# Performance work log

Hardware: AMD Instinct MI355X
Metric: run time of the kernel (lower is better)

The kernel has to match this reference:

```python
import jax, jax.numpy as jnp
import numpy as np

B, C, H, W = 4, 256, 64, 64
CQ = C // 8


def setup_inputs() -> dict:
    key = jax.random.key(0)
    ks = jax.random.split(key, 7)
    x = jax.random.normal(ks[0], (B, C, H, W), dtype=jnp.float32)
    Wq = jax.random.normal(ks[1], (CQ, C), dtype=jnp.float32) * 0.02
    bq = jnp.zeros((CQ,), dtype=jnp.float32)
    Wk = jax.random.normal(ks[2], (CQ, C), dtype=jnp.float32) * 0.02
    bk = jnp.zeros((CQ,), dtype=jnp.float32)
    Wv = jax.random.normal(ks[3], (C, C), dtype=jnp.float32) * 0.02
    bv = jnp.zeros((C,), dtype=jnp.float32)
    return {"x": x, "Wq": Wq, "bq": bq, "Wk": Wk, "bk": bk, "Wv": Wv, "bv": bv}


def reference(x, Wq, bq, Wk, bk, Wv, bv):
    b, c, h, w = x.shape
    n = h * w
    xf = x.reshape(b, c, n)                                   # [B,C,N]
    # 1x1 convs are per-pixel GEMMs
    q = jnp.einsum('qc,bcn->bnq', Wq, xf) + bq                # [B,N,Cq]
    k = jnp.einsum('qc,bcn->bqn', Wk, xf) + bk[None, :, None] # [B,Cq,N]
    v = jnp.einsum('vc,bcn->bnv', Wv, xf) + bv                # [B,N,C]
    scale = float(n) ** 0.5
    energy = jnp.einsum('bnq,bqm->bnm', q, k) / scale         # [B,N,N]
    attn = jax.nn.softmax(energy, axis=-1)
    out = jnp.einsum('bnm,bmv->bnv', attn, v)                 # [B,N,C]
    # Faithful to torch's out.view(B,C,H,W) applied to the contiguous [B,N,C]
    # tensor: a raw memory reinterpretation, NOT a transpose.
    return out.reshape(b, c, h, w)
```

## Files before the change

### kernel.cpp

```cpp
#include <hip/hip_runtime.h>

#define BATCH 4
#define CH    256
#define NPIX  4096
#define CQD   32

typedef __bf16 bf16;
typedef bf16 bf16x8 __attribute__((ext_vector_type(8)));
typedef bf16 bf16x4 __attribute__((ext_vector_type(4)));
typedef float f32x4 __attribute__((ext_vector_type(4)));

#define MFMA16 __builtin_amdgcn_mfma_f32_16x16x32_bf16

__global__ __launch_bounds__(256) void proj_kernel(
    const float* __restrict__ x,
    const float* __restrict__ Wq, const float* __restrict__ bq,
    const float* __restrict__ Wk, const float* __restrict__ bk,
    const float* __restrict__ Wv, const float* __restrict__ bv,
    bf16* __restrict__ qp, bf16* __restrict__ kp, bf16* __restrict__ vT)
{
    __shared__ __align__(16) bf16 xT[32][264];
    __shared__ __align__(16) bf16 vstage[4][16][40];

    const int t  = threadIdx.x;
    const int b  = blockIdx.x >> 7;
    const int n0 = (blockIdx.x & 127) << 5;
    const int w    = t >> 6;
    const int lane = t & 63;
    const int l16  = t & 15;
    const int quad = (t & 63) >> 4;

    auto params = [&](int rt, const float*& Wp, const float*& bp, float& scale,
                      int& rbase, int& kind) {
        int ro = w * 80 + rt * 16;
        if (ro < 32)      { Wp = Wq; bp = bq; scale = 0.015625f; rbase = ro;      kind = 0; }
        else if (ro < 64) { Wp = Wk; bp = bk; scale = 1.0f;      rbase = ro - 32; kind = 1; }
        else              { Wp = Wv; bp = bv; scale = 1.0f;      rbase = ro - 64; kind = 2; }
    };

    const float* Wp; const float* bp; float scale; int rbase; int kind;
    params(0, Wp, bp, scale, rbase, kind);
    float4 wraw[16];
    {
        const float* wrow = Wp + (size_t)(rbase + l16) * CH + quad * 8;
#pragma unroll
        for (int kc = 0; kc < 8; ++kc) {
            wraw[2 * kc]     = *(const float4*)(wrow + kc * 32);
            wraw[2 * kc + 1] = *(const float4*)(wrow + kc * 32 + 4);
        }
    }

    const float* xb = x + (size_t)b * CH * NPIX;
#pragma unroll
    for (int j = 0; j < 8; ++j) {
        int id = t + j * 256;
        int c  = id >> 3;
        int n4 = (id & 7) << 2;
        float4 vv = *(const float4*)(xb + (size_t)c * NPIX + n0 + n4);
        xT[n4 + 0][c] = (bf16)vv.x;
        xT[n4 + 1][c] = (bf16)vv.y;
        xT[n4 + 2][c] = (bf16)vv.z;
        xT[n4 + 3][c] = (bf16)vv.w;
    }
    __syncthreads();

    for (int rt = 0; rt < 5; ++rt) {
        bf16x8 afrag[8];
#pragma unroll
        for (int kc = 0; kc < 8; ++kc) {
            float4 wa = wraw[2 * kc], wb = wraw[2 * kc + 1];
            bf16x8 a;
            a[0] = (bf16)wa.x; a[1] = (bf16)wa.y; a[2] = (bf16)wa.z; a[3] = (bf16)wa.w;
            a[4] = (bf16)wb.x; a[5] = (bf16)wb.y; a[6] = (bf16)wb.z; a[7] = (bf16)wb.w;
            afrag[kc] = a;
        }
        const float* Wp2; const float* bp2; float scale2; int rbase2; int kind2;
        if (rt < 4) {
            params(rt + 1, Wp2, bp2, scale2, rbase2, kind2);
            const float* wrow = Wp2 + (size_t)(rbase2 + l16) * CH + quad * 8;
#pragma unroll
            for (int kc = 0; kc < 8; ++kc) {
                wraw[2 * kc]     = *(const float4*)(wrow + kc * 32);
                wraw[2 * kc + 1] = *(const float4*)(wrow + kc * 32 + 4);
            }
        }
        float bv4[4];
#pragma unroll
        for (int r = 0; r < 4; ++r) bv4[r] = bp[rbase + quad * 4 + r];

#pragma unroll
        for (int nt = 0; nt < 2; ++nt) {
            f32x4 acc = {0.f, 0.f, 0.f, 0.f};
#pragma unroll
            for (int kc = 0; kc < 8; ++kc) {
                bf16x8 bfr = *(const bf16x8*)&xT[nt * 16 + l16][kc * 32 + quad * 8];
                acc = MFMA16(afrag[kc], bfr, acc, 0, 0, 0);
            }
            if (kind != 2) {
                bf16x4 pk;
#pragma unroll
                for (int r = 0; r < 4; ++r)
                    pk[r] = (bf16)((acc[r] + bv4[r]) * scale);
                int n = n0 + nt * 16 + l16;
                bf16* dst = (kind == 0) ? qp : kp;
                *(bf16x4*)&dst[((size_t)b * NPIX + n) * CQD + rbase + quad * 4] = pk;
            } else {
#pragma unroll
                for (int r = 0; r < 4; ++r)
                    vstage[w][quad * 4 + r][nt * 16 + l16] = (bf16)(acc[r] + bv4[r]);
            }
        }
        if (kind == 2) {
            int vrow = lane >> 2, vcc = lane & 3;
            bf16x8 chunk = *(const bf16x8*)&vstage[w][vrow][vcc * 8];
            *(bf16x8*)&vT[((size_t)b * CH + rbase + vrow) * NPIX + n0 + vcc * 8] = chunk;
        }
        if (rt < 4) { Wp = Wp2; bp = bp2; scale = scale2; rbase = rbase2; kind = kind2; }
    }
}

template<int S, bool DIRECT>
__global__ __launch_bounds__(256, 2) void attn_kernel(
    const bf16* __restrict__ qp, const bf16* __restrict__ kp,
    const bf16* __restrict__ vT,
    bf16* __restrict__ Opart, float* __restrict__ Lpart,
    float* __restrict__ out)
{
    __shared__ __align__(16) bf16 Kt[64][40];
    __shared__ __align__(16) bf16 Vt[256][64];
    __shared__ __align__(16) bf16 Pb[4][16][72];

    const int t    = threadIdx.x;
    const int bid  = blockIdx.x;
    const int s    = bid % S;
    const int tq   = bid / S;
    const int b    = tq >> 5;
    const int qt   = tq & 31;
    const int n0   = qt << 7;
    const int w    = t >> 6;
    const int lane = t & 63;
    const int l16  = t & 15;
    const int quad = (t & 63) >> 4;

    const bf16* qpb = qp + ((size_t)b * NPIX + n0 + w * 32) * CQD;
    bf16x8 qfrag[2];
    qfrag[0] = *(const bf16x8*)(qpb + (size_t)l16 * CQD + quad * 8);
    qfrag[1] = *(const bf16x8*)(qpb + (size_t)(16 + l16) * CQD + quad * 8);

    f32x4 o[2][16];
#pragma unroll
    for (int g = 0; g < 2; ++g)
#pragma unroll
        for (int ct = 0; ct < 16; ++ct) o[g][ct] = (f32x4){0.f, 0.f, 0.f, 0.f};
    float lsum[2] = {0.f, 0.f};

    const bf16* kpb = kp + (size_t)b * NPIX * CQD;
    const bf16* vTb = vT + (size_t)b * CH * NPIX;
    const int k0 = s * (NPIX / S);
    const int sw = l16 & 7;

    for (int mi = 0; mi < NPIX / S / 64; ++mi) {
        const int m0 = k0 + (mi << 6);
        {
            int row = t >> 2, cc = t & 3;
            *(bf16x8*)&Kt[row][cc * 8] =
                *(const bf16x8*)(kpb + (size_t)(m0 + row) * CQD + cc * 8);
        }
#pragma unroll
        for (int j = 0; j < 8; ++j) {
            int id  = t + j * 256;
            int row = id >> 3, cc = id & 7;
            *(bf16x8*)&Vt[row][(cc ^ (row & 7)) * 8] =
                *(const bf16x8*)(vTb + (size_t)row * NPIX + m0 + cc * 8);
        }
        __syncthreads();

        f32x4 sv[2][4];
#pragma unroll
        for (int mt = 0; mt < 4; ++mt) {
            bf16x8 kfrag = *(const bf16x8*)&Kt[mt * 16 + l16][quad * 8];
            f32x4 z = {0.f, 0.f, 0.f, 0.f};
            sv[0][mt] = MFMA16(kfrag, qfrag[0], z, 0, 0, 0);
            sv[1][mt] = MFMA16(kfrag, qfrag[1], z, 0, 0, 0);
        }

        bf16x8 pf[2][2];
#pragma unroll
        for (int g = 0; g < 2; ++g) {
            float rs = 0.f;
#pragma unroll
            for (int mt = 0; mt < 4; ++mt) {
                bf16x4 pk;
#pragma unroll
                for (int r = 0; r < 4; ++r) {
                    float e = __expf(sv[g][mt][r]);
                    rs += e;
                    pk[r] = (bf16)e;
                }
                *(bf16x4*)&Pb[w][l16][mt * 16 + quad * 4] = pk;
            }
            lsum[g] += rs;
#pragma unroll
            for (int kc = 0; kc < 2; ++kc)
                pf[g][kc] = *(const bf16x8*)&Pb[w][l16][kc * 32 + quad * 8];
        }

#pragma unroll
        for (int ct = 0; ct < 16; ++ct) {
            int row = ct * 16 + l16;
            bf16x8 v0 = *(const bf16x8*)&Vt[row][((quad) ^ sw) * 8];
            bf16x8 v1 = *(const bf16x8*)&Vt[row][((4 + quad) ^ sw) * 8];
            o[0][ct] = MFMA16(pf[0][0], v0, o[0][ct], 0, 0, 0);
            o[0][ct] = MFMA16(pf[0][1], v1, o[0][ct], 0, 0, 0);
            o[1][ct] = MFMA16(pf[1][0], v0, o[1][ct], 0, 0, 0);
            o[1][ct] = MFMA16(pf[1][1], v1, o[1][ct], 0, 0, 0);
        }
        __syncthreads();
    }

    float l_g[2];
#pragma unroll
    for (int g = 0; g < 2; ++g) {
        float v = lsum[g];
        v += __shfl_xor(v, 16);
        v += __shfl_xor(v, 32);
        l_g[g] = v;
    }

    if (!DIRECT) {
        const size_t prb = (((size_t)s * BATCH + b) * 32 + qt) * 128 + w * 32;
        if (quad == 0) {
#pragma unroll
            for (int g = 0; g < 2; ++g)
                Lpart[prb + g * 16 + l16] = l_g[g];
        }
#pragma unroll
        for (int g = 0; g < 2; ++g) {
            float rinv[4];
#pragma unroll
            for (int r = 0; r < 4; ++r) rinv[r] = 1.0f / __shfl(l_g[g], quad * 4 + r);
#pragma unroll
            for (int h = 0; h < 4; ++h) {
#pragma unroll
                for (int c2 = 0; c2 < 4; ++c2) {
                    int ct = h * 4 + c2;
#pragma unroll
                    for (int r = 0; r < 4; ++r)
                        Pb[w][quad * 4 + r][c2 * 16 + l16] = (bf16)(o[g][ct][r] * rinv[r]);
                }
                int vrow = lane >> 3, vcc = lane & 7;
#pragma unroll
                for (int pass = 0; pass < 2; ++pass) {
                    bf16x8 chunk = *(const bf16x8*)&Pb[w][pass * 8 + vrow][vcc * 8];
                    *(bf16x8*)&Opart[(prb + g * 16 + pass * 8 + vrow) * CH +
                                     h * 64 + vcc * 8] = chunk;
                }
            }
        }
    } else {
        float* ob = out + ((size_t)b * NPIX + n0 + w * 32) * CH;
#pragma unroll
        for (int g = 0; g < 2; ++g) {
            float rinv[4];
#pragma unroll
            for (int r = 0; r < 4; ++r) rinv[r] = 1.0f / __shfl(l_g[g], quad * 4 + r);
#pragma unroll
            for (int ct = 0; ct < 16; ++ct)
#pragma unroll
                for (int r = 0; r < 4; ++r)
                    ob[(size_t)(g * 16 + quad * 4 + r) * CH + ct * 16 + l16] =
                        o[g][ct][r] * rinv[r];
        }
    }
}

template<int S>
__global__ __launch_bounds__(256) void combine_kernel(
    const bf16* __restrict__ Opart, const float* __restrict__ Lpart,
    float* __restrict__ out)
{
    int idx  = blockIdx.x * 256 + threadIdx.x;
    int nrow = idx >> 5;
    int cc   = (idx & 31) * 8;
    int b    = nrow >> 12, nin = nrow & 4095;
    int qt   = nin >> 7,  rl  = nin & 127;

    size_t pr[S];
    float  ls[S], wsum = 0.f;
#pragma unroll
    for (int s = 0; s < S; ++s) {
        pr[s] = (((size_t)s * BATCH + b) * 32 + qt) * 128 + rl;
        ls[s] = Lpart[pr[s]];
        wsum += ls[s];
    }
    float inv = 1.0f / wsum;

    float acc[8] = {0.f, 0.f, 0.f, 0.f, 0.f, 0.f, 0.f, 0.f};
#pragma unroll
    for (int s = 0; s < S; ++s) {
        bf16x8 ov = *(const bf16x8*)&Opart[pr[s] * CH + cc];
        float wn = ls[s] * inv;
#pragma unroll
        for (int j = 0; j < 8; ++j) acc[j] += wn * (float)ov[j];
    }
    float4 o0 = {acc[0], acc[1], acc[2], acc[3]};
    float4 o1 = {acc[4], acc[5], acc[6], acc[7]};
    *(float4*)&out[(size_t)nrow * CH + cc]     = o0;
    *(float4*)&out[(size_t)nrow * CH + cc + 4] = o1;
}

extern "C" void kernel_launch(void* const* d_in, const int* in_sizes, int n_in,
                              void* d_out, int out_size, void* d_ws, size_t ws_size,
                              hipStream_t stream) {
    const float* x  = (const float*)d_in[0];
    const float* Wq = (const float*)d_in[1];
    const float* bq = (const float*)d_in[2];
    const float* Wk = (const float*)d_in[3];
    const float* bk = (const float*)d_in[4];
    const float* Wv = (const float*)d_in[5];
    const float* bv = (const float*)d_in[6];
    float* out = (float*)d_out;

    char* ws = (char*)d_ws;
    const size_t qpB   = (size_t)BATCH * NPIX * CQD * 2;
    const size_t vTB   = (size_t)BATCH * CH * NPIX * 2;
    const size_t baseB = 2 * qpB + vTB;
    const size_t oprtB = (size_t)BATCH * NPIX * CH * 2;
    const size_t mlB   = (size_t)BATCH * NPIX * 4;

    bf16* qp = (bf16*)ws;
    bf16* kp = (bf16*)(ws + qpB);
    bf16* vT = (bf16*)(ws + 2 * qpB);

    proj_kernel<<<dim3(BATCH * (NPIX / 32)), dim3(256), 0, stream>>>(
        x, Wq, bq, Wk, bk, Wv, bv, qp, kp, vT);

    auto need = [&](int S) { return baseB + (size_t)S * (oprtB + mlB); };
    int S = (ws_size >= need(4)) ? 4 : (ws_size >= need(2)) ? 2
          : (ws_size >= need(1)) ? 1 : 0;

    if (S > 0) {
        bf16*  Opart = (bf16*)(ws + baseB);
        float* Lpart = (float*)(ws + baseB + (size_t)S * oprtB);
        if (S == 4) {
            attn_kernel<4, false><<<dim3(128 * 4), dim3(256), 0, stream>>>(
                qp, kp, vT, Opart, Lpart, out);
            combine_kernel<4><<<dim3(2048), dim3(256), 0, stream>>>(Opart, Lpart, out);
        } else if (S == 2) {
            attn_kernel<2, false><<<dim3(128 * 2), dim3(256), 0, stream>>>(
                qp, kp, vT, Opart, Lpart, out);
            combine_kernel<2><<<dim3(2048), dim3(256), 0, stream>>>(Opart, Lpart, out);
        } else {
            attn_kernel<1, false><<<dim3(128), dim3(256), 0, stream>>>(
                qp, kp, vT, Opart, Lpart, out);
            combine_kernel<1><<<dim3(2048), dim3(256), 0, stream>>>(Opart, Lpart, out);
        }
    } else {
        attn_kernel<1, true><<<dim3(128), dim3(256), 0, stream>>>(
            qp, kp, vT, nullptr, nullptr, out);
    }
}
```

Measured before the change: 175.5 us.

## Double-buffer V tiles via async global-to-LDS loads and restructure projection tiling

The attention kernel now double-buffers the V tile in LDS and fills it with global_load_lds direct copies, while K fragments are prefetched into registers for the next iteration. This overlaps the memory fetch with the MFMA work and removes the separate K staging in LDS. The P buffer gets an XOR-swizzled layout to cut bank conflicts. The projection kernel switches to 64-pixel tiles with each block computing half of the output rows, and it loads weights directly instead of prefetching them. The changes raise LDS use and rely on correct lane-to-address mapping for the LDS DMA path.

```diff
diff --git a/kernel.cpp b/kernel.cpp
--- a/kernel.cpp
+++ b/kernel.cpp
@@ -12,50 +12,36 @@
 
 #define MFMA16 __builtin_amdgcn_mfma_f32_16x16x32_bf16
 
-__global__ __launch_bounds__(256) void proj_kernel(
+#define GLOAD_LDS16(g, l) __builtin_amdgcn_global_load_lds( \
+    (const __attribute__((address_space(1))) void*)(g),     \
+    (__attribute__((address_space(3))) void*)(l), 16, 0, 0)
+
+__global__ __launch_bounds__(256, 2) void proj_kernel(
     const float* __restrict__ x,
     const float* __restrict__ Wq, const float* __restrict__ bq,
     const float* __restrict__ Wk, const float* __restrict__ bk,
     const float* __restrict__ Wv, const float* __restrict__ bv,
     bf16* __restrict__ qp, bf16* __restrict__ kp, bf16* __restrict__ vT)
 {
-    __shared__ __align__(16) bf16 xT[32][264];
-    __shared__ __align__(16) bf16 vstage[4][16][40];
-
-    const int t  = threadIdx.x;
-    const int b  = blockIdx.x >> 7;
-    const int n0 = (blockIdx.x & 127) << 5;
+    __shared__ __align__(16) bf16 xT[64][264];
+    __shared__ __align__(16) bf16 vstage[4][16][72];
+
+    const int t    = threadIdx.x;
+    const int b    = blockIdx.x >> 7;
+    const int rem  = blockIdx.x & 127;
+    const int n0   = (rem >> 1) << 6;
+    const int half = rem & 1;
     const int w    = t >> 6;
     const int lane = t & 63;
     const int l16  = t & 15;
     const int quad = (t & 63) >> 4;
 
-    auto params = [&](int rt, const float*& Wp, const float*& bp, float& scale,
-                      int& rbase, int& kind) {
-        int ro = w * 80 + rt * 16;
-        if (ro < 32)      { Wp = Wq; bp = bq; scale = 0.015625f; rbase = ro;      kind = 0; }
-        else if (ro < 64) { Wp = Wk; bp = bk; scale = 1.0f;      rbase = ro - 32; kind = 1; }
-        else              { Wp = Wv; bp = bv; scale = 1.0f;      rbase = ro - 64; kind = 2; }
-    };
-
-    const float* Wp; const float* bp; float scale; int rbase; int kind;
-    params(0, Wp, bp, scale, rbase, kind);
-    float4 wraw[16];
-    {
-        const float* wrow = Wp + (size_t)(rbase + l16) * CH + quad * 8;
-#pragma unroll
-        for (int kc = 0; kc < 8; ++kc) {
-            wraw[2 * kc]     = *(const float4*)(wrow + kc * 32);
-            wraw[2 * kc + 1] = *(const float4*)(wrow + kc * 32 + 4);
-        }
-    }
-
     const float* xb = x + (size_t)b * CH * NPIX;
 #pragma unroll
-    for (int j = 0; j < 8; ++j) {
+    for (int j = 0; j < 16; ++j) {
         int id = t + j * 256;
-        int c  = id >> 3;
-        int n4 = (id & 7) << 2;
+        int c  = id >> 4;
+        int n4 = (id & 15) << 2;
         float4 vv = *(const float4*)(xb + (size_t)c * NPIX + n0 + n4);
         xT[n4 + 0][c] = (bf16)vv.x;
         xT[n4 + 1][c] = (bf16)vv.y;
@@ -64,32 +50,30 @@
     }
     __syncthreads();
 
-    for (int rt = 0; rt < 5; ++rt) {
+    for (int tt = w; tt < 10; tt += 4) {
+        int ro = half * 160 + tt * 16;
+        const float* Wp; const float* bp; float scale; int rbase; int kind;
+        if (ro < 32)      { Wp = Wq; bp = bq; scale = 0.015625f; rbase = ro;      kind = 0; }
+        else if (ro < 64) { Wp = Wk; bp = bk; scale = 1.0f;      rbase = ro - 32; kind = 1; }
+        else              { Wp = Wv; bp = bv; scale = 1.0f;      rbase = ro - 64; kind = 2; }
+
         bf16x8 afrag[8];
+        const float* wrow = Wp + (size_t)(rbase + l16) * CH + quad * 8;
 #pragma unroll
         for (int kc = 0; kc < 8; ++kc) {
-            float4 wa = wraw[2 * kc], wb = wraw[2 * kc + 1];
+            float4 wa = *(const float4*)(wrow + kc * 32);
+            float4 wb = *(const float4*)(wrow + kc * 32 + 4);
             bf16x8 a;
             a[0] = (bf16)wa.x; a[1] = (bf16)wa.y; a[2] = (bf16)wa.z; a[3] = (bf16)wa.w;
             a[4] = (bf16)wb.x; a[5] = (bf16)wb.y; a[6] = (bf16)wb.z; a[7] = (bf16)wb.w;
             afrag[kc] = a;
         }
-        const float* Wp2; const float* bp2; float scale2; int rbase2; int kind2;
-        if (rt < 4) {
-            params(rt + 1, Wp2, bp2, scale2, rbase2, kind2);
-            const float* wrow = Wp2 + (size_t)(rbase2 + l16) * CH + quad * 8;
-#pragma unroll
-            for (int kc = 0; kc < 8; ++kc) {
-                wraw[2 * kc]     = *(const float4*)(wrow + kc * 32);
-                wraw[2 * kc + 1] = *(const float4*)(wrow + kc * 32 + 4);
-            }
-        }
         float bv4[4];
 #pragma unroll
         for (int r = 0; r < 4; ++r) bv4[r] = bp[rbase + quad * 4 + r];
 
 #pragma unroll
-        for (int nt = 0; nt < 2; ++nt) {
+        for (int nt = 0; nt < 4; ++nt) {
             f32x4 acc = {0.f, 0.f, 0.f, 0.f};
 #pragma unroll
             for (int kc = 0; kc < 8; ++kc) {
@@ -111,11 +95,14 @@
             }
         }
         if (kind == 2) {
-            int vrow = lane >> 2, vcc = lane & 3;
-            bf16x8 chunk = *(const bf16x8*)&vstage[w][vrow][vcc * 8];
-            *(bf16x8*)&vT[((size_t)b * CH + rbase + vrow) * NPIX + n0 + vcc * 8] = chunk;
-        }
-        if (rt < 4) { Wp = Wp2; bp = bp2; scale = scale2; rbase = rbase2; kind = kind2; }
+            int vrow = lane >> 3, vcc = lane & 7;
+#pragma unroll
+            for (int pass = 0; pass < 2; ++pass) {
+                bf16x8 chunk = *(const bf16x8*)&vstage[w][pass * 8 + vrow][vcc * 8];
+                *(bf16x8*)&vT[((size_t)b * CH + rbase + pass * 8 + vrow) * NPIX +
+                              n0 + vcc * 8] = chunk;
+            }
+        }
     }
 }
 
@@ -126,9 +113,8 @@
     bf16* __restrict__ Opart, float* __restrict__ Lpart,
     float* __restrict__ out)
 {
-    __shared__ __align__(16) bf16 Kt[64][40];
-    __shared__ __align__(16) bf16 Vt[256][64];
-    __shared__ __align__(16) bf16 Pb[4][16][72];
+    __shared__ __align__(16) bf16 Vt[2][256][64];
+    __shared__ __align__(16) bf16 Pb[4][2][16][64];
 
     const int t    = threadIdx.x;
     const int bid  = blockIdx.x;
@@ -141,6 +127,7 @@
     const int lane = t & 63;
     const int l16  = t & 15;
     const int quad = (t & 63) >> 4;
+    const int sw   = l16 & 7;
 
     const bf16* qpb = qp + ((size_t)b * NPIX + n0 + w * 32) * CQD;
     bf16x8 qfrag[2];
@@ -157,34 +144,44 @@
     const bf16* kpb = kp + (size_t)b * NPIX * CQD;
     const bf16* vTb = vT + (size_t)b * CH * NPIX;
     const int k0 = s * (NPIX / S);
-    const int sw = l16 & 7;
-
-    for (int mi = 0; mi < NPIX / S / 64; ++mi) {
-        const int m0 = k0 + (mi << 6);
-        {
-            int row = t >> 2, cc = t & 3;
-            *(bf16x8*)&Kt[row][cc * 8] =
-                *(const bf16x8*)(kpb + (size_t)(m0 + row) * CQD + cc * 8);
-        }
+    const int iters = NPIX / S / 64;
+
+    const int vrow_off = lane >> 3;
+    const int vchunk   = (lane & 7) ^ vrow_off;
+    auto issue_vt = [&](int buf, int m0) {
 #pragma unroll
         for (int j = 0; j < 8; ++j) {
-            int id  = t + j * 256;
-            int row = id >> 3, cc = id & 7;
-            *(bf16x8*)&Vt[row][(cc ^ (row & 7)) * 8] =
-                *(const bf16x8*)(vTb + (size_t)row * NPIX + m0 + cc * 8);
-        }
-        __syncthreads();
+            int rowbase = j * 32 + w * 8;
+            const bf16* src = vTb + (size_t)(rowbase + vrow_off) * NPIX + m0 + vchunk * 8;
+            GLOAD_LDS16(src, &Vt[buf][rowbase][0]);
+        }
+    };
+    auto load_kf = [&](int m0, bf16x8* kf) {
+#pragma unroll
+        for (int mt = 0; mt < 4; ++mt)
+            kf[mt] = *(const bf16x8*)(kpb + (size_t)(m0 + mt * 16 + l16) * CQD + quad * 8);
+    };
+
+    bf16x8 kfa[4], kfb[4];
+    issue_vt(0, k0);
+    load_kf(k0, kfa);
+    __syncthreads();
+
+    for (int mi = 0; mi < iters; ++mi) {
+        const int cur = mi & 1;
+        if (mi + 1 < iters) {
+            issue_vt(cur ^ 1, k0 + ((mi + 1) << 6));
+            load_kf(k0 + ((mi + 1) << 6), kfb);
+        }
 
         f32x4 sv[2][4];
 #pragma unroll
         for (int mt = 0; mt < 4; ++mt) {
-            bf16x8 kfrag = *(const bf16x8*)&Kt[mt * 16 + l16][quad * 8];
             f32x4 z = {0.f, 0.f, 0.f, 0.f};
-            sv[0][mt] = MFMA16(kfrag, qfrag[0], z, 0, 0, 0);
-            sv[1][mt] = MFMA16(kfrag, qfrag[1], z, 0, 0, 0);
-        }
-
-        bf16x8 pf[2][2];
+            sv[0][mt] = MFMA16(kfa[mt], qfrag[0], z, 0, 0, 0);
+            sv[1][mt] = MFMA16(kfa[mt], qfrag[1], z, 0, 0, 0);
+        }
+
 #pragma unroll
         for (int g = 0; g < 2; ++g) {
             float rs = 0.f;
@@ -197,25 +194,33 @@
                     rs += e;
                     pk[r] = (bf16)e;
                 }
-                *(bf16x4*)&Pb[w][l16][mt * 16 + quad * 4] = pk;
+                int slot = (2 * mt + (quad >> 1)) ^ sw;
+                *(bf16x4*)&Pb[w][g][l16][slot * 8 + (quad & 1) * 4] = pk;
             }
             lsum[g] += rs;
-#pragma unroll
-            for (int kc = 0; kc < 2; ++kc)
-                pf[g][kc] = *(const bf16x8*)&Pb[w][l16][kc * 32 + quad * 8];
-        }
+        }
+        bf16x8 pf[2][2];
+#pragma unroll
+        for (int g = 0; g < 2; ++g)
+#pragma unroll
+            for (int kc = 0; kc < 2; ++kc) {
+                int slot = (4 * kc + quad) ^ sw;
+                pf[g][kc] = *(const bf16x8*)&Pb[w][g][l16][slot * 8];
+            }
 
 #pragma unroll
         for (int ct = 0; ct < 16; ++ct) {
             int row = ct * 16 + l16;
-            bf16x8 v0 = *(const bf16x8*)&Vt[row][((quad) ^ sw) * 8];
-            bf16x8 v1 = *(const bf16x8*)&Vt[row][((4 + quad) ^ sw) * 8];
+            bf16x8 v0 = *(const bf16x8*)&Vt[cur][row][((quad) ^ sw) * 8];
+            bf16x8 v1 = *(const bf16x8*)&Vt[cur][row][((4 + quad) ^ sw) * 8];
             o[0][ct] = MFMA16(pf[0][0], v0, o[0][ct], 0, 0, 0);
             o[0][ct] = MFMA16(pf[0][1], v1, o[0][ct], 0, 0, 0);
             o[1][ct] = MFMA16(pf[1][0], v0, o[1][ct], 0, 0, 0);
             o[1][ct] = MFMA16(pf[1][1], v1, o[1][ct], 0, 0, 0);
         }
         __syncthreads();
+#pragma unroll
+        for (int i = 0; i < 4; ++i) kfa[i] = kfb[i];
     }
 
     float l_g[2];
@@ -234,6 +239,7 @@
             for (int g = 0; g < 2; ++g)
                 Lpart[prb + g * 16 + l16] = l_g[g];
         }
+        bf16* eb = &Pb[w][0][0][0];
 #pragma unroll
         for (int g = 0; g < 2; ++g) {
             float rinv[4];
@@ -246,12 +252,13 @@
                     int ct = h * 4 + c2;
 #pragma unroll
                     for (int r = 0; r < 4; ++r)
-                        Pb[w][quad * 4 + r][c2 * 16 + l16] = (bf16)(o[g][ct][r] * rinv[r]);
+                        eb[(quad * 4 + r) * 72 + c2 * 16 + l16] =
+                            (bf16)(o[g][ct][r] * rinv[r]);
                 }
                 int vrow = lane >> 3, vcc = lane & 7;
 #pragma unroll
                 for (int pass = 0; pass < 2; ++pass) {
-                    bf16x8 chunk = *(const bf16x8*)&Pb[w][pass * 8 + vrow][vcc * 8];
+                    bf16x8 chunk = *(const bf16x8*)&eb[(pass * 8 + vrow) * 72 + vcc * 8];
                     *(bf16x8*)&Opart[(prb + g * 16 + pass * 8 + vrow) * CH +
                                      h * 64 + vcc * 8] = chunk;
                 }
@@ -332,7 +339,7 @@
     bf16* kp = (bf16*)(ws + qpB);
     bf16* vT = (bf16*)(ws + 2 * qpB);
 
-    proj_kernel<<<dim3(BATCH * (NPIX / 32)), dim3(256), 0, stream>>>(
+    proj_kernel<<<dim3(BATCH * 64 * 2), dim3(256), 0, stream>>>(
         x, Wq, bq, Wk, bk, Wv, bv, qp, kp, vT);
 
     auto need = [&](int S) { return baseB + (size_t)S * (oprtB + mlB); };
```

New measurement: 145.1 us. 17.3% less time.
